# Performance work log

Hardware: AMD Instinct MI355X
Metric: run time of the kernel (lower is better)

The kernel has to match this reference:

```python
import jax, jax.numpy as jnp
import numpy as np

MAX_LEN = 20
MIN_LEN = 3


def setup_inputs() -> dict:
    key = jax.random.key(0)
    ks = jax.random.split(key, 7)
    B, latent, hidden, out = 8192, 256, 512, 512
    in_dim = latent + (MAX_LEN - MIN_LEN)  # 273: one-hot length code + noise

    def w(k, shape, fan_in):
        return jax.random.normal(k, shape, jnp.float32) * (1.0 / np.sqrt(fan_in))

    return {
        "x": jax.random.normal(ks[0], (B, latent), jnp.float32),
        "W1": w(ks[1], (hidden, in_dim), in_dim), "b1": jnp.zeros(hidden, jnp.float32),
        "W2": w(ks[2], (hidden, hidden), hidden), "b2": jnp.zeros(hidden, jnp.float32),
        "W3": w(ks[3], (out, hidden), hidden), "b3": jnp.zeros(out, jnp.float32),
        "Wih": w(ks[4], (4 * out, out), out), "Whh": w(ks[5], (4 * out, out), out),
        "bih": jnp.zeros(4 * out, jnp.float32), "bhh": jnp.zeros(4 * out, jnp.float32),
        "sentence_len": 16,
    }


def reference(x, W1, b1, W2, b2, W3, b3, Wih, Whh, bih, bhh, sentence_len):
    B = x.shape[0]
    out = W3.shape[0]
    # length one-hot (deterministic part of forward)
    onehot = jnp.zeros((B, MAX_LEN - MIN_LEN), x.dtype).at[:, MAX_LEN - sentence_len].set(1.0)
    z = jnp.concatenate([onehot, x], axis=1)  # [B, 273]
    h = jax.nn.relu(z @ W1.T + b1)
    h = jax.nn.relu(h @ W2.T + b2)
    x0 = jax.nn.sigmoid(h @ W3.T + b3)  # [B, out] first LSTM input

    bias = bih + bhh
    h0 = jnp.zeros((B, out), x.dtype)
    c0 = jnp.zeros((B, out), x.dtype)

    def step(carry, _):
        inp, h, c = carry
        gates = inp @ Wih.T + h @ Whh.T + bias  # [B, 4*out], torch order i,f,g,o
        i, f, g, o = jnp.split(gates, 4, axis=1)
        c_new = jax.nn.sigmoid(f) * c + jax.nn.sigmoid(i) * jnp.tanh(g)
        h_new = jax.nn.sigmoid(o) * jnp.tanh(c_new)
        # next input is this step's output (the module feeds h_n back in)
        return (h_new, h_new, c_new), h_new

    _, hs = jax.lax.scan(step, (x0, h0, c0), None, length=sentence_len)  # [T, B, out]
    return jnp.transpose(hs, (1, 0, 2))  # [B, T, out]
```

## Files before the change

### kernel.cpp

```cpp
#include <hip/hip_runtime.h>
#include <hip/hip_bf16.h>

typedef __attribute__((ext_vector_type(8))) short s8v;
typedef __attribute__((ext_vector_type(4))) float f4v;

__device__ __forceinline__ void gl_lds16(const void* g, void* l) {
  __builtin_amdgcn_global_load_lds(
      (const __attribute__((address_space(1))) unsigned int*)g,
      (__attribute__((address_space(3))) unsigned int*)l, 16, 0, 0);
}

__device__ __forceinline__ unsigned short f2b(float v) {
  __hip_bfloat16 b = __float2bfloat16(v);
  return __builtin_bit_cast(unsigned short, b);
}

__device__ __forceinline__ float sigm(float x) {
  float e = __builtin_amdgcn_exp2f(-1.442695041f * x);
  return __builtin_amdgcn_rcpf(1.0f + e);
}
__device__ __forceinline__ float tanh_f(float x) {
  float e = __builtin_amdgcn_exp2f(-2.885390082f * x);
  return __builtin_fmaf(2.0f, __builtin_amdgcn_rcpf(1.0f + e), -1.0f);
}


__global__ void k_conv_bf16(const float* __restrict__ src, unsigned short* __restrict__ dst, int n) {
  int i = blockIdx.x * blockDim.x + threadIdx.x;
  if (i < n) dst[i] = f2b(src[i]);
}

__global__ void k_prep_w1(const float* __restrict__ W1, const float* __restrict__ b1,
                          const int* __restrict__ slen,
                          unsigned short* __restrict__ W1x, float* __restrict__ b1e) {
  int i = blockIdx.x * blockDim.x + threadIdx.x;
  if (i < 512 * 256) {
    int n = i >> 8, k = i & 255;
    W1x[i] = f2b(W1[n * 273 + 17 + k]);
  }
  if (i < 512) {
    int col = 20 - *slen;
    b1e[i] = b1[i] + W1[i * 273 + col];
  }
}

__global__ void k_prep_gates(const float* __restrict__ Wih, const float* __restrict__ Whh,
                             const float* __restrict__ bih, const float* __restrict__ bhh,
                             unsigned short* __restrict__ Wihb, unsigned short* __restrict__ Wsum,
                             float* __restrict__ biasg) {
  int i = blockIdx.x * blockDim.x + threadIdx.x;
  if (i < 2048 * 512) {
    float a = Wih[i];
    Wihb[i] = f2b(a);
    Wsum[i] = f2b(a + Whh[i]);
  }
  if (i < 2048) biasg[i] = bih[i] + bhh[i];
}


template <int ACT>
__global__ __launch_bounds__(256)
void k_gemm_bt(const unsigned short* __restrict__ A, const unsigned short* __restrict__ Bt,
               const float* __restrict__ bias, unsigned short* __restrict__ C,
               int M, int N, int K) {
  __shared__ __align__(16) unsigned short As[128 * 32];
  __shared__ __align__(16) unsigned short Bs[128 * 32];
  const int tid = threadIdx.x;
  const int m0 = blockIdx.y * 128, n0 = blockIdx.x * 128;
  const int lane = tid & 63, wave = tid >> 6;
  const int wm = (wave >> 1) * 64, wn = (wave & 1) * 64;
  const int lr = lane & 15, lq = lane >> 4;

  f4v acc[4][4];
#pragma unroll
  for (int i = 0; i < 4; ++i)
#pragma unroll
    for (int j = 0; j < 4; ++j) acc[i][j] = (f4v){0.f, 0.f, 0.f, 0.f};

  for (int k0 = 0; k0 < K; k0 += 32) {
    __syncthreads();
#pragma unroll
    for (int s = 0; s < 2; ++s) {
      int cc = tid + s * 256;
      int row = cc >> 2, kk = (cc & 3) << 3;
      gl_lds16(&A[(long)(m0 + row) * K + k0 + kk], &As[cc * 8]);
      gl_lds16(&Bt[(long)(n0 + row) * K + k0 + kk], &Bs[cc * 8]);
    }
    __syncthreads();

    s8v a[4], b[4];
#pragma unroll
    for (int i = 0; i < 4; ++i)
      a[i] = *(const s8v*)&As[(wm + i * 16 + lr) * 32 + lq * 8];
#pragma unroll
    for (int j = 0; j < 4; ++j)
      b[j] = *(const s8v*)&Bs[(wn + j * 16 + lr) * 32 + lq * 8];
#pragma unroll
    for (int i = 0; i < 4; ++i)
#pragma unroll
      for (int j = 0; j < 4; ++j)
        acc[i][j] = __builtin_amdgcn_mfma_f32_16x16x32_bf16(a[i], b[j], acc[i][j], 0, 0, 0);
  }

#pragma unroll
  for (int i = 0; i < 4; ++i) {
#pragma unroll
    for (int j = 0; j < 4; ++j) {
#pragma unroll
      for (int r = 0; r < 4; ++r) {
        int m = m0 + wm + i * 16 + lq * 4 + r;
        int n = n0 + wn + j * 16 + lr;
        float v = acc[i][j][r] + bias[n];
        v = (ACT == 0) ? fmaxf(v, 0.0f) : sigm(v);
        C[(long)m * N + n] = f2b(v);
      }
    }
  }
}


__global__ __launch_bounds__(256, 4)
void k_lstm_step2(const unsigned short* __restrict__ A,
                  const unsigned short* __restrict__ Wg,
                  const float* __restrict__ bias,
                  float* __restrict__ Cst,
                  unsigned short* __restrict__ Hout,
                  float* __restrict__ Out,
                  int T, int t, int first) {
  __shared__ __align__(16) unsigned short As[2][128 * 32];
  __shared__ __align__(16) unsigned short Bs[2][4 * 32 * 32];
  const int tid = threadIdx.x;
  const int p = blockIdx.x;
  const int q = p >> 3;
  const int mt = (p & 7) + ((q & 7) << 3);
  const int nt = q >> 3;
  const long m0 = (long)mt * 128;
  const int n0 = nt * 32;
  const int lane = tid & 63, wave = tid >> 6;
  const int lr = lane & 15, lq = lane >> 4;
  const int wr = (wave >> 1) * 64;
  const int wu = (wave & 1) * 16;

  f4v acc[4][4];
#pragma unroll
  for (int g = 0; g < 4; ++g)
#pragma unroll
    for (int i = 0; i < 4; ++i) acc[g][i] = (f4v){0.f, 0.f, 0.f, 0.f};

  auto stage = [&](int sel, int kt) {
#pragma unroll
    for (int s = 0; s < 2; ++s) {
      int c = tid + s * 256;
      int row = c >> 2, kk = (c & 3) << 3;
      gl_lds16(&A[(m0 + row) * 512 + kt * 32 + kk], &As[sel][c * 8]);
    }
#pragma unroll
    for (int s = 0; s < 2; ++s) {
      int c = tid + s * 256;
      int g = c >> 7, idx = c & 127;
      int row = idx >> 2, kk = (idx & 3) << 3;
      gl_lds16(&Wg[((long)(g * 512 + n0 + row)) * 512 + kt * 32 + kk], &Bs[sel][c * 8]);
    }
  };

  stage(0, 0);
  __syncthreads();

  int sel = 0;
  for (int kt = 0; kt < 16; ++kt) {
    if (kt < 15) stage(sel ^ 1, kt + 1);

    s8v a[4], b[4];
#pragma unroll
    for (int i = 0; i < 4; ++i)
      a[i] = *(const s8v*)&As[sel][(wr + i * 16 + lr) * 32 + lq * 8];
#pragma unroll
    for (int g = 0; g < 4; ++g)
      b[g] = *(const s8v*)&Bs[sel][g * 1024 + (wu + lr) * 32 + lq * 8];
#pragma unroll
    for (int g = 0; g < 4; ++g)
#pragma unroll
      for (int i = 0; i < 4; ++i)
        acc[g][i] = __builtin_amdgcn_mfma_f32_16x16x32_bf16(a[i], b[g], acc[g][i], 0, 0, 0);

    if (kt < 15) {
      __syncthreads();
      sel ^= 1;
    }
  }

#pragma unroll
  for (int i = 0; i < 4; ++i) {
#pragma unroll
    for (int r = 0; r < 4; ++r) {
      long m = m0 + wr + i * 16 + lq * 4 + r;
      int u = n0 + wu + lr;
      float gi = acc[0][i][r] + bias[u];
      float gf = acc[1][i][r] + bias[512 + u];
      float gg = acc[2][i][r] + bias[1024 + u];
      float go = acc[3][i][r] + bias[1536 + u];
      float c_old = first ? 0.0f : Cst[m * 512 + u];
      float cn = sigm(gf) * c_old + sigm(gi) * tanh_f(gg);
      float h = sigm(go) * tanh_f(cn);
      Cst[m * 512 + u] = cn;
      Hout[m * 512 + u] = f2b(h);
      __builtin_nontemporal_store(h, &Out[(m * T + t) * 512 + u]);
    }
  }
}


extern "C" void kernel_launch(void* const* d_in, const int* in_sizes, int n_in,
                              void* d_out, int out_size, void* d_ws, size_t ws_size,
                              hipStream_t stream) {
  const float* x   = (const float*)d_in[0];
  const float* W1  = (const float*)d_in[1];
  const float* b1  = (const float*)d_in[2];
  const float* W2  = (const float*)d_in[3];
  const float* b2  = (const float*)d_in[4];
  const float* W3  = (const float*)d_in[5];
  const float* b3  = (const float*)d_in[6];
  const float* Wih = (const float*)d_in[7];
  const float* Whh = (const float*)d_in[8];
  const float* bih = (const float*)d_in[9];
  const float* bhh = (const float*)d_in[10];
  const int* slen  = (const int*)d_in[11];
  float* out = (float*)d_out;

  const int B = in_sizes[0] / 256;
  const int T = out_size / (B * 512);

  size_t o = 0;
  auto alloc = [&](size_t bytes) {
    o = (o + 255) & ~(size_t)255;
    void* r = (char*)d_ws + o;
    o += bytes;
    return r;
  };
  unsigned short* xb    = (unsigned short*)alloc((size_t)B * 256 * 2);
  unsigned short* W1x   = (unsigned short*)alloc(512 * 256 * 2);
  unsigned short* W2b   = (unsigned short*)alloc(512 * 512 * 2);
  unsigned short* W3b   = (unsigned short*)alloc(512 * 512 * 2);
  unsigned short* Wihb  = (unsigned short*)alloc(2048 * 512 * 2);
  unsigned short* Wsumb = (unsigned short*)alloc(2048 * 512 * 2);
  float* b1e   = (float*)alloc(512 * 4);
  float* biasg = (float*)alloc(2048 * 4);
  unsigned short* h1 = (unsigned short*)alloc((size_t)B * 512 * 2);
  unsigned short* h2 = (unsigned short*)alloc((size_t)B * 512 * 2);
  float* cbuf = (float*)alloc((size_t)B * 512 * 4);
  (void)ws_size;

  k_conv_bf16<<<(B * 256 + 255) / 256, 256, 0, stream>>>(x, xb, B * 256);
  k_conv_bf16<<<(512 * 512 + 255) / 256, 256, 0, stream>>>(W2, W2b, 512 * 512);
  k_conv_bf16<<<(512 * 512 + 255) / 256, 256, 0, stream>>>(W3, W3b, 512 * 512);
  k_prep_w1<<<(512 * 256 + 255) / 256, 256, 0, stream>>>(W1, b1, slen, W1x, b1e);
  k_prep_gates<<<(2048 * 512 + 255) / 256, 256, 0, stream>>>(Wih, Whh, bih, bhh, Wihb, Wsumb,
                                                             biasg);

  k_gemm_bt<0><<<dim3(4, B / 128), 256, 0, stream>>>(xb, W1x, b1e, h1, B, 512, 256);
  k_gemm_bt<0><<<dim3(4, B / 128), 256, 0, stream>>>(h1, W2b, b2, h2, B, 512, 512);
  k_gemm_bt<1><<<dim3(4, B / 128), 256, 0, stream>>>(h2, W3b, b3, h1, B, 512, 512);

  for (int t = 0; t < T; ++t) {
    const unsigned short* a = (t % 2 == 0) ? h1 : h2;
    unsigned short* ho      = (t % 2 == 0) ? h2 : h1;
    k_lstm_step2<<<dim3(1024), 256, 0, stream>>>(
        a, (t == 0) ? Wihb : Wsumb, biasg, cbuf, ho, out, T, t, (t == 0) ? 1 : 0);
  }
}
```

Before: 741.4 us.

## Load LSTM step operands directly from global memory into registers, drop LDS staging

The LSTM step kernel stops double-buffering A and gate-weight tiles through shared memory and instead has each lane load its MFMA fragments straight from global memory, with the K loop fully unrolled. This removes the LDS writes, LDS reads and per-iteration barriers. In exchange, each 16-byte fragment load is a strided global access that relies on L1/L2 for reuse across waves, and the extra loads in flight may raise register pressure. Bias values are also hoisted out of the epilogue loop.

```diff
diff --git a/kernel.cpp b/kernel.cpp
--- a/kernel.cpp
+++ b/kernel.cpp
@@ -120,15 +120,13 @@
 
 
 __global__ __launch_bounds__(256, 4)
-void k_lstm_step2(const unsigned short* __restrict__ A,
+void k_lstm_step3(const unsigned short* __restrict__ A,
                   const unsigned short* __restrict__ Wg,
                   const float* __restrict__ bias,
                   float* __restrict__ Cst,
                   unsigned short* __restrict__ Hout,
                   float* __restrict__ Out,
                   int T, int t, int first) {
-  __shared__ __align__(16) unsigned short As[2][128 * 32];
-  __shared__ __align__(16) unsigned short Bs[2][4 * 32 * 32];
   const int tid = threadIdx.x;
   const int p = blockIdx.x;
   const int q = p >> 3;
@@ -141,64 +139,49 @@
   const int wr = (wave >> 1) * 64;
   const int wu = (wave & 1) * 16;
 
+  const unsigned short* ap[4];
+  const unsigned short* bp[4];
+#pragma unroll
+  for (int i = 0; i < 4; ++i)
+    ap[i] = A + (m0 + wr + i * 16 + lr) * 512 + lq * 8;
+#pragma unroll
+  for (int g = 0; g < 4; ++g)
+    bp[g] = Wg + ((long)(g * 512 + n0 + wu + lr)) * 512 + lq * 8;
+
   f4v acc[4][4];
 #pragma unroll
   for (int g = 0; g < 4; ++g)
 #pragma unroll
     for (int i = 0; i < 4; ++i) acc[g][i] = (f4v){0.f, 0.f, 0.f, 0.f};
 
-  auto stage = [&](int sel, int kt) {
-#pragma unroll
-    for (int s = 0; s < 2; ++s) {
-      int c = tid + s * 256;
-      int row = c >> 2, kk = (c & 3) << 3;
-      gl_lds16(&A[(m0 + row) * 512 + kt * 32 + kk], &As[sel][c * 8]);
-    }
-#pragma unroll
-    for (int s = 0; s < 2; ++s) {
-      int c = tid + s * 256;
-      int g = c >> 7, idx = c & 127;
-      int row = idx >> 2, kk = (idx & 3) << 3;
-      gl_lds16(&Wg[((long)(g * 512 + n0 + row)) * 512 + kt * 32 + kk], &Bs[sel][c * 8]);
-    }
-  };
-
-  stage(0, 0);
-  __syncthreads();
-
-  int sel = 0;
+#pragma unroll
   for (int kt = 0; kt < 16; ++kt) {
-    if (kt < 15) stage(sel ^ 1, kt + 1);
-
     s8v a[4], b[4];
 #pragma unroll
-    for (int i = 0; i < 4; ++i)
-      a[i] = *(const s8v*)&As[sel][(wr + i * 16 + lr) * 32 + lq * 8];
-#pragma unroll
-    for (int g = 0; g < 4; ++g)
-      b[g] = *(const s8v*)&Bs[sel][g * 1024 + (wu + lr) * 32 + lq * 8];
+    for (int i = 0; i < 4; ++i) a[i] = *(const s8v*)(ap[i] + kt * 32);
+#pragma unroll
+    for (int g = 0; g < 4; ++g) b[g] = *(const s8v*)(bp[g] + kt * 32);
 #pragma unroll
     for (int g = 0; g < 4; ++g)
 #pragma unroll
       for (int i = 0; i < 4; ++i)
         acc[g][i] = __builtin_amdgcn_mfma_f32_16x16x32_bf16(a[i], b[g], acc[g][i], 0, 0, 0);
-
-    if (kt < 15) {
-      __syncthreads();
-      sel ^= 1;
-    }
-  }
-
+  }
+
+  const int u = n0 + wu + lr;
+  const float b_i = bias[u];
+  const float b_f = bias[512 + u];
+  const float b_g = bias[1024 + u];
+  const float b_o = bias[1536 + u];
 #pragma unroll
   for (int i = 0; i < 4; ++i) {
 #pragma unroll
     for (int r = 0; r < 4; ++r) {
       long m = m0 + wr + i * 16 + lq * 4 + r;
-      int u = n0 + wu + lr;
-      float gi = acc[0][i][r] + bias[u];
-      float gf = acc[1][i][r] + bias[512 + u];
-      float gg = acc[2][i][r] + bias[1024 + u];
-      float go = acc[3][i][r] + bias[1536 + u];
+      float gi = acc[0][i][r] + b_i;
+      float gf = acc[1][i][r] + b_f;
+      float gg = acc[2][i][r] + b_g;
+      float go = acc[3][i][r] + b_o;
       float c_old = first ? 0.0f : Cst[m * 512 + u];
       float cn = sigm(gf) * c_old + sigm(gi) * tanh_f(gg);
       float h = sigm(go) * tanh_f(cn);
@@ -264,7 +247,7 @@
   for (int t = 0; t < T; ++t) {
     const unsigned short* a = (t % 2 == 0) ? h1 : h2;
     unsigned short* ho      = (t % 2 == 0) ? h2 : h1;
-    k_lstm_step2<<<dim3(1024), 256, 0, stream>>>(
+    k_lstm_step3<<<dim3(1024), 256, 0, stream>>>(
         a, (t == 0) ? Wihb : Wsumb, biasg, cbuf, ho, out, T, t, (t == 0) ? 1 : 0);
   }
 }
```

Measured after the change: 1.376 ms. 85.6% more time.
